# Kernel optimization log

Hardware: AMD Instinct MI355X
Metric: run time of the kernel (lower is better)

Reference implementation:

```python
import jax, jax.numpy as jnp
import numpy as np

D_MODEL = 1024
NUM_HEADS = 16
ROPE_THETA = 10000.0


def setup_inputs() -> dict:
    key = jax.random.key(0)
    ks = jax.random.split(key, 5)
    B, S, D = 4, 2048, D_MODEL
    std = (2.0 / (D * D)) ** 0.5
    return {
        "x": jax.random.normal(ks[0], (B, S, D), dtype=jnp.float32),
        "Wq": jax.random.normal(ks[1], (D, D), dtype=jnp.float32) * std,
        "Wk": jax.random.normal(ks[2], (D, D), dtype=jnp.float32) * std,
        "Wv": jax.random.normal(ks[3], (D, D), dtype=jnp.float32) * std,
        "Wo": jax.random.normal(ks[4], (D, D), dtype=jnp.float32) * std,
    }


def _apply_rope(t, sin, cos):
    # t: [B, H, S, d_k]; sin/cos: [S, d_k//2] (broadcast over B, H)
    e = t[..., 0::2]
    o = t[..., 1::2]
    rot = jnp.stack((e * cos - o * sin, e * sin + o * cos), axis=-1)
    return rot.reshape(t.shape)  # interleave back to d_k


def reference(x, Wq, Wk, Wv, Wo):
    B, S, D = x.shape
    H = NUM_HEADS
    dk = D // H

    def proj(W):
        y = jnp.einsum('bsd,ed->bse', x, W)  # Linear: weight is [out, in]
        return y.reshape(B, S, H, dk).transpose(0, 2, 1, 3)  # [B,H,S,dk]

    q, k, v = proj(Wq), proj(Wk), proj(Wv)

    # RoPE cache (token_positions = arange(S))
    half = dk // 2
    inv_freq = 1.0 / (ROPE_THETA ** (jnp.arange(half, dtype=jnp.float32) * 2.0 / dk))
    angles = jnp.arange(S, dtype=jnp.float32)[:, None] * inv_freq[None, :]  # [S, half]
    sin, cos = jnp.sin(angles), jnp.cos(angles)
    q = _apply_rope(q, sin, cos)
    k = _apply_rope(k, sin, cos)

    # scaled dot-product attention with causal mask
    scores = jnp.einsum('bhqd,bhkd->bhqk', q, k) / jnp.sqrt(jnp.float32(dk))
    causal = jnp.tril(jnp.ones((S, S), dtype=bool))
    scores = jnp.where(causal, scores, jnp.finfo(scores.dtype).min)
    p = jax.nn.softmax(scores, axis=-1)
    out = jnp.einsum('bhqk,bhkd->bhqd', p, v)  # [B,H,S,dk]

    out = out.transpose(0, 2, 1, 3).reshape(B, S, D)
    return jnp.einsum('bsd,ed->bse', out, Wo)
```

## Files before the change

kernel.cpp:

```cpp
#include <hip/hip_runtime.h>

typedef unsigned short u16;
typedef unsigned int   u32;

typedef short    short8 __attribute__((ext_vector_type(8)));
typedef __bf16   bf16x8 __attribute__((ext_vector_type(8)));
typedef _Float16 half8  __attribute__((ext_vector_type(8)));
typedef float    f32x4  __attribute__((ext_vector_type(4)));

#define S_LEN   2048
#define DM      1024
#define NHEAD   16
#define DK      64
#define BH_TOT  64
#define M_TOK   8192
#define KDIM    1024

__device__ __forceinline__ u16 f2bf(float f) {
    u32 u = __builtin_bit_cast(u32, f);
    u += 0x7FFFu + ((u >> 16) & 1u);
    return (u16)(u >> 16);
}
__device__ __forceinline__ float bf2f(u16 h) {
    u32 u = ((u32)h) << 16;
    return __builtin_bit_cast(float, u);
}
__device__ __forceinline__ f32x4 mfma_bf16(short8 a, short8 b, f32x4 c) {
    return __builtin_amdgcn_mfma_f32_16x16x32_bf16(
        __builtin_bit_cast(bf16x8, a), __builtin_bit_cast(bf16x8, b), c, 0, 0, 0);
}
__device__ __forceinline__ f32x4 mfma_f16(half8 a, half8 b, f32x4 c) {
    return __builtin_amdgcn_mfma_f32_16x16x32_f16(a, b, c, 0, 0, 0);
}
__device__ __forceinline__ u32 pk_f16(float a, float b) {
    return __builtin_bit_cast(u32, __builtin_amdgcn_cvt_pkrtz(a, b));
}
__device__ __forceinline__ void gl_lds16(const void* g, void* l) {
    __builtin_amdgcn_global_load_lds(
        (const __attribute__((address_space(1))) u32*)g,
        (__attribute__((address_space(3))) u32*)l, 16, 0, 0);
}
__device__ __forceinline__ void bar_raw() { asm volatile("s_barrier" ::: "memory"); }
__device__ __forceinline__ void wait_vm4() { asm volatile("s_waitcnt vmcnt(4)" ::: "memory"); }
__device__ __forceinline__ void wait_vm0() { asm volatile("s_waitcnt vmcnt(0)" ::: "memory"); }

__device__ __forceinline__ int perm_inv(int rc) {
    const int nt = rc >> 4, mid = (rc >> 2) & 3, r = rc & 3;
    return 32 * (nt >> 1) + 8 * mid + 4 * (nt & 1) + r;
}

__global__ void cvt_all(const float4* __restrict__ x,  const float4* __restrict__ Wq,
                        const float4* __restrict__ Wk, const float4* __restrict__ Wv,
                        const float4* __restrict__ Wo,
                        uint2* __restrict__ oX, uint2* __restrict__ oWcat,
                        uint2* __restrict__ oWo) {
    const int i = blockIdx.x * 256 + threadIdx.x;
    const float4* in;
    uint2* out;
    if (i < 2097152) {
        in = x + i;  out = oX + i;
    } else {
        const int j = i - 2097152;
        const int w = j >> 18, k = j & 262143;
        in  = (w == 0 ? Wq : w == 1 ? Wk : w == 2 ? Wv : Wo) + k;
        out = (w < 3) ? (oWcat + w * 262144 + k) : (oWo + k);
    }
    float4 f = *in;
    uint2 o;
    o.x = (u32)f2bf(f.x) | ((u32)f2bf(f.y) << 16);
    o.y = (u32)f2bf(f.z) | ((u32)f2bf(f.w) << 16);
    *out = o;
}

template <int MODE>
__global__ __launch_bounds__(256)
void gemm_nt(const u16* __restrict__ A, const u16* __restrict__ Bw,
             u16* __restrict__ oQ, u16* __restrict__ oK, u16* __restrict__ oVt,
             float* __restrict__ oF) {
    __shared__ u16 As[2][128 * 32];
    __shared__ u16 Bs[2][128 * 32];
    const int tid  = threadIdx.x;
    const int wave = tid >> 6, lane = tid & 63;
    const int quad = lane >> 4, l15 = lane & 15;
    const int wr = wave >> 1, wc = wave & 1;
    const int mbase = blockIdx.y * 128;
    const int nbase = blockIdx.x * 128;

    f32x4 acc[4][4];
#pragma unroll
    for (int i = 0; i < 4; i++)
#pragma unroll
        for (int j = 0; j < 4; j++) acc[i][j] = (f32x4)0.0f;

    const int srow0 = wave * 32 + (lane >> 2);
    const int srow1 = srow0 + 16;
    const int scolb = ((lane & 3) ^ ((lane >> 3) & 3)) * 16;
    const int ldsOff = wave * 2048 + lane * 16;
    const u16* gA0 = A  + (size_t)(mbase + srow0) * KDIM;
    const u16* gA1 = A  + (size_t)(mbase + srow1) * KDIM;
    const u16* gB0 = Bw + (size_t)(nbase + srow0) * KDIM;
    const u16* gB1 = Bw + (size_t)(nbase + srow1) * KDIM;
    const int koffq = (quad ^ ((l15 >> 1) & 3)) * 8;

    gl_lds16((const char*)gA0 + scolb, (char*)As[0] + ldsOff);
    gl_lds16((const char*)gA1 + scolb, (char*)As[0] + ldsOff + 1024);
    gl_lds16((const char*)gB0 + scolb, (char*)Bs[0] + ldsOff);
    gl_lds16((const char*)gB1 + scolb, (char*)Bs[0] + ldsOff + 1024);

    const int KT = KDIM / 32;
    for (int kt = 0; kt < KT; kt++) {
        const int cur = kt & 1, nxt = cur ^ 1;
        const int kkn = ((kt + 1 < KT) ? (kt + 1) : kt) * 32;
        bar_raw();
        gl_lds16((const char*)(gA0 + kkn) + scolb, (char*)As[nxt] + ldsOff);
        gl_lds16((const char*)(gA1 + kkn) + scolb, (char*)As[nxt] + ldsOff + 1024);
        gl_lds16((const char*)(gB0 + kkn) + scolb, (char*)Bs[nxt] + ldsOff);
        gl_lds16((const char*)(gB1 + kkn) + scolb, (char*)Bs[nxt] + ldsOff + 1024);
        wait_vm4();
        bar_raw();

        short8 af[4], bf[4];
#pragma unroll
        for (int mt = 0; mt < 4; mt++)
            af[mt] = *(const short8*)&As[cur][(wr * 64 + mt * 16 + l15) * 32 + koffq];
#pragma unroll
        for (int nt = 0; nt < 4; nt++)
            bf[nt] = *(const short8*)&Bs[cur][(wc * 64 + nt * 16 + l15) * 32 + koffq];
#pragma unroll
        for (int mt = 0; mt < 4; mt++)
#pragma unroll
            for (int nt = 0; nt < 4; nt++)
                acc[mt][nt] = mfma_bf16(af[mt], bf[nt], acc[mt][nt]);
    }
    wait_vm0();

    const int proj_blk = (MODE == 0) ? (nbase >> 10) : 2;

    float fq[4], cf[4], sf[4];
    if (MODE == 0 && proj_blk < 2) {
#pragma unroll
        for (int nt = 0; nt < 4; nt++) {
            const float fi = __expf(-(float)(nt * 8 + (l15 >> 1)) * 0.287823136624255f);
            fq[nt] = fi;
            cf[nt] = cosf(fi);
            sf[nt] = sinf(fi);
        }
    }
    const int par = l15 & 1;

#pragma unroll
    for (int mt = 0; mt < 4; mt++) {
#pragma unroll
        for (int nt = 0; nt < 4; nt++) {
            const int n  = nbase + wc * 64 + nt * 16 + l15;
            const int mb = mbase + wr * 64 + mt * 16 + quad * 4;
            f32x4 v = acc[mt][nt];
            if (MODE == 0) {
                const int e = n & 1023;
                const int h = e >> 6, d = e & 63;
                if (proj_blk == 2) {
                    const int b_ = mb >> 11, s = mb & 2047;
                    const int bh = b_ * NHEAD + h;
                    uint2 pk;
                    pk.x = pk_f16(v[0], v[1]);
                    pk.y = pk_f16(v[2], v[3]);
                    *(uint2*)&oVt[((size_t)bh * DK + d) * S_LEN + s] = pk;
                } else {
                    u16* dst = (proj_blk == 0) ? oQ : oK;
                    float vp[4];
#pragma unroll
                    for (int r = 0; r < 4; r++) vp[r] = __shfl_xor(v[r], 1);
                    const int b_ = mb >> 11, s0 = mb & 2047;
                    const int bh = b_ * NHEAD + h;
                    float cc = cosf((float)s0 * fq[nt]);
                    float ss = sinf((float)s0 * fq[nt]);
#pragma unroll
                    for (int r = 0; r < 4; r++) {
                        const float res = par ? (vp[r] * ss + v[r] * cc)
                                              : (v[r] * cc - vp[r] * ss);
                        dst[((size_t)bh * S_LEN + (s0 + r)) * DK + d] = f2bf(res);
                        const float c2 = cc * cf[nt] - ss * sf[nt];
                        ss = ss * cf[nt] + cc * sf[nt];
                        cc = c2;
                    }
                }
            } else {
#pragma unroll
                for (int r = 0; r < 4; r++)
                    oF[(size_t)(mb + r) * DM + n] = v[r];
            }
        }
    }
}

__global__ __launch_bounds__(256)
void flash_attn(const u16* __restrict__ Q, const u16* __restrict__ K,
                const u16* __restrict__ Vt, u16* __restrict__ Oc) {
    __shared__ u16 Ks[2][64 * 64];
    __shared__ u16 Vs[2][64 * 64];
    const int qt = 31 - (int)blockIdx.y;
    const int bh = blockIdx.x;
    const int tid  = threadIdx.x;
    const int wave = tid >> 6, lane = tid & 63;
    const int quad = lane >> 4, l15 = lane & 15;
    const int x7 = l15 & 7;
    const size_t headQK = (size_t)bh * S_LEN * DK;
    const size_t headVt = (size_t)bh * DK * S_LEN;
    const int b = bh >> 4, h = bh & 15;
    const float SCL = 0.18033688011112042f;

    half8 ones;
#pragma unroll
    for (int j = 0; j < 8; j++) ones[j] = (_Float16)1.0f;

    const int rwl  = lane >> 3;
    const int scol = (lane & 7) ^ rwl;
    const int rc0 = wave * 16 + rwl, rc1 = rc0 + 8;
    const u16* gK0 = K  + headQK + (size_t)perm_inv(rc0) * DK + scol * 8;
    const u16* gK1 = K  + headQK + (size_t)perm_inv(rc1) * DK + scol * 8;
    const u16* gV0 = Vt + headVt + (size_t)rc0 * S_LEN + scol * 8;
    const u16* gV1 = Vt + headVt + (size_t)rc1 * S_LEN + scol * 8;
    const int ldsOff = wave * 2048 + lane * 16;
    const int koff0 = (quad ^ x7) * 8;
    const int koff1 = ((4 + quad) ^ x7) * 8;

    const int qrow = qt * 64 + wave * 16 + l15;
    const short8 qf0 = *(const short8*)&Q[headQK + (size_t)qrow * DK + quad * 8];
    const short8 qf1 = *(const short8*)&Q[headQK + (size_t)qrow * DK + 32 + quad * 8];

    float m_st = -__builtin_inff();
    f32x4 lacc = (f32x4)0.0f;
    f32x4 oacc[4];
#pragma unroll
    for (int n = 0; n < 4; n++) oacc[n] = (f32x4)0.0f;

    gl_lds16(gK0, (char*)Ks[0] + ldsOff);
    gl_lds16(gK1, (char*)Ks[0] + ldsOff + 1024);
    gl_lds16(gV0, (char*)Vs[0] + ldsOff);
    gl_lds16(gV1, (char*)Vs[0] + ldsOff + 1024);

    for (int kt = 0; kt <= qt; kt++) {
        const int cur = kt & 1, nxt = cur ^ 1;
        bar_raw();
        {
            const int ktn = (kt < qt) ? kt + 1 : qt;
            gl_lds16(gK0 + (size_t)ktn * 64 * DK, (char*)Ks[nxt] + ldsOff);
            gl_lds16(gK1 + (size_t)ktn * 64 * DK, (char*)Ks[nxt] + ldsOff + 1024);
            gl_lds16(gV0 + ktn * 64,              (char*)Vs[nxt] + ldsOff);
            gl_lds16(gV1 + ktn * 64,              (char*)Vs[nxt] + ldsOff + 1024);
        }
        wait_vm4();
        bar_raw();

        f32x4 sc[4];
#pragma unroll
        for (int nt = 0; nt < 4; nt++) {
            const int rb = (nt * 16 + l15) * 64;
            short8 kf0 = *(const short8*)&Ks[cur][rb + koff0];
            short8 kf1 = *(const short8*)&Ks[cur][rb + koff1];
            f32x4 z = (f32x4)0.0f;
            z = mfma_bf16(kf0, qf0, z);
            z = mfma_bf16(kf1, qf1, z);
#pragma unroll
            for (int r = 0; r < 4; r++) z[r] *= SCL;
            sc[nt] = z;
        }
        if (kt == qt) {
            const int qloc = wave * 16 + l15;
#pragma unroll
            for (int nt = 0; nt < 4; nt++) {
                const int kb = 32 * (nt >> 1) + 8 * quad + 4 * (nt & 1);
#pragma unroll
                for (int r = 0; r < 4; r++)
                    if (kb + r > qloc) sc[nt][r] = -__builtin_inff();
            }
        }
        float mx0 = fmaxf(fmaxf(sc[0][0], sc[0][1]), fmaxf(sc[0][2], sc[0][3]));
        float mx1 = fmaxf(fmaxf(sc[1][0], sc[1][1]), fmaxf(sc[1][2], sc[1][3]));
        float mx2 = fmaxf(fmaxf(sc[2][0], sc[2][1]), fmaxf(sc[2][2], sc[2][3]));
        float mx3 = fmaxf(fmaxf(sc[3][0], sc[3][1]), fmaxf(sc[3][2], sc[3][3]));
        float mx = fmaxf(fmaxf(mx0, mx1), fmaxf(mx2, mx3));
        mx = fmaxf(mx, __shfl_xor(mx, 16));
        mx = fmaxf(mx, __shfl_xor(mx, 32));
        const float mn = fmaxf(m_st, mx);
        const float alpha = __builtin_amdgcn_exp2f(m_st - mn);
        m_st = mn;
#pragma unroll
        for (int nt = 0; nt < 4; nt++)
#pragma unroll
            for (int r = 0; r < 4; r++)
                sc[nt][r] = __builtin_amdgcn_exp2f(sc[nt][r] - m_st);
        u32 pw[8];
        pw[0] = pk_f16(sc[0][0], sc[0][1]); pw[1] = pk_f16(sc[0][2], sc[0][3]);
        pw[2] = pk_f16(sc[1][0], sc[1][1]); pw[3] = pk_f16(sc[1][2], sc[1][3]);
        pw[4] = pk_f16(sc[2][0], sc[2][1]); pw[5] = pk_f16(sc[2][2], sc[2][3]);
        pw[6] = pk_f16(sc[3][0], sc[3][1]); pw[7] = pk_f16(sc[3][2], sc[3][3]);
        half8 pf0 = __builtin_bit_cast(half8, *(uint4*)&pw[0]);
        half8 pf1 = __builtin_bit_cast(half8, *(uint4*)&pw[4]);
        float alr[4];
#pragma unroll
        for (int r = 0; r < 4; r++) alr[r] = __shfl(alpha, quad * 20 + r);
#pragma unroll
        for (int n = 0; n < 4; n++)
#pragma unroll
            for (int r = 0; r < 4; r++) oacc[n][r] *= alr[r];
#pragma unroll
        for (int r = 0; r < 4; r++) lacc[r] *= alr[r];
#pragma unroll
        for (int c = 0; c < 2; c++) {
            const half8 pf = c ? pf1 : pf0;
            lacc = mfma_f16(pf, ones, lacc);
            const int voff = ((c * 4 + quad) ^ x7) * 8;
#pragma unroll
            for (int nt2 = 0; nt2 < 4; nt2++) {
                half8 vf = __builtin_bit_cast(half8,
                    *(const short8*)&Vs[cur][(nt2 * 16 + l15) * 64 + voff]);
                oacc[nt2] = mfma_f16(pf, vf, oacc[nt2]);
            }
        }
    }
    wait_vm0();

#pragma unroll
    for (int r = 0; r < 4; r++) {
        const float inv = 1.0f / lacc[r];
        const int s = qt * 64 + wave * 16 + quad * 4 + r;
#pragma unroll
        for (int nt2 = 0; nt2 < 4; nt2++)
            Oc[((size_t)(b * S_LEN + s)) * DM + h * 64 + nt2 * 16 + l15] =
                f2bf(oacc[nt2][r] * inv);
    }
}

#define OFF_XBF  ((size_t)0)
#define OFF_WCAT ((size_t)8388608)
#define OFF_WO   ((size_t)11534336)
#define OFF_QB   ((size_t)12582912)
#define OFF_KB   ((size_t)20971520)
#define OFF_VT   ((size_t)29360128)

extern "C" void kernel_launch(void* const* d_in, const int* in_sizes, int n_in,
                              void* d_out, int out_size, void* d_ws, size_t ws_size,
                              hipStream_t stream) {
    const float* x  = (const float*)d_in[0];
    const float* Wq = (const float*)d_in[1];
    const float* Wk = (const float*)d_in[2];
    const float* Wv = (const float*)d_in[3];
    const float* Wo = (const float*)d_in[4];
    u16* ws  = (u16*)d_ws;
    u16* XBF = ws + OFF_XBF;
    u16* WCA = ws + OFF_WCAT;
    u16* WOB = ws + OFF_WO;
    u16* QB  = ws + OFF_QB;
    u16* KB  = ws + OFF_KB;
    u16* VT  = ws + OFF_VT;
    u16* AT  = XBF;

    cvt_all<<<12288, 256, 0, stream>>>((const float4*)x, (const float4*)Wq,
                                       (const float4*)Wk, (const float4*)Wv,
                                       (const float4*)Wo,
                                       (uint2*)XBF, (uint2*)WCA, (uint2*)WOB);

    gemm_nt<0><<<dim3(24, 64), 256, 0, stream>>>(XBF, WCA, QB, KB, VT, nullptr);
    flash_attn<<<dim3(64, 32), 256, 0, stream>>>(QB, KB, VT, AT);
    gemm_nt<1><<<dim3(8, 64), 256, 0, stream>>>(AT, WOB, nullptr, nullptr, nullptr,
                                                (float*)d_out);
}
```

Measured before the change: 277.2 us.

## Process two query tiles per flash block and precompute RoPE sin/cos table

Each flash-attention block now handles 128 query rows as two 64-row halves that share every K/V tile loaded into LDS. This halves the grid and the number of K/V loads per query. Separately, the RoPE sin/cos values are precomputed into a workspace table inside the conversion kernel, and the QKV GEMM epilogue loads them instead of running the sin/cos recurrence. The trade-offs are higher register pressure from doubled accumulators, fewer blocks for causal load balancing, and extra global reads in the epilogue.

```diff
diff --git a/kernel.cpp b/kernel.cpp
--- a/kernel.cpp
+++ b/kernel.cpp
@@ -21,10 +21,6 @@
     u += 0x7FFFu + ((u >> 16) & 1u);
     return (u16)(u >> 16);
 }
-__device__ __forceinline__ float bf2f(u16 h) {
-    u32 u = ((u32)h) << 16;
-    return __builtin_bit_cast(float, u);
-}
 __device__ __forceinline__ f32x4 mfma_bf16(short8 a, short8 b, f32x4 c) {
     return __builtin_amdgcn_mfma_f32_16x16x32_bf16(
         __builtin_bit_cast(bf16x8, a), __builtin_bit_cast(bf16x8, b), c, 0, 0, 0);
@@ -53,30 +49,40 @@
                         const float4* __restrict__ Wk, const float4* __restrict__ Wv,
                         const float4* __restrict__ Wo,
                         uint2* __restrict__ oX, uint2* __restrict__ oWcat,
-                        uint2* __restrict__ oWo) {
+                        uint2* __restrict__ oWo,
+                        float* __restrict__ sT, float* __restrict__ cT) {
     const int i = blockIdx.x * 256 + threadIdx.x;
-    const float4* in;
-    uint2* out;
-    if (i < 2097152) {
-        in = x + i;  out = oX + i;
+    if (i < 3145728) {
+        const float4* in;
+        uint2* out;
+        if (i < 2097152) {
+            in = x + i;  out = oX + i;
+        } else {
+            const int j = i - 2097152;
+            const int w = j >> 18, k = j & 262143;
+            in  = (w == 0 ? Wq : w == 1 ? Wk : w == 2 ? Wv : Wo) + k;
+            out = (w < 3) ? (oWcat + w * 262144 + k) : (oWo + k);
+        }
+        float4 f = *in;
+        uint2 o;
+        o.x = (u32)f2bf(f.x) | ((u32)f2bf(f.y) << 16);
+        o.y = (u32)f2bf(f.z) | ((u32)f2bf(f.w) << 16);
+        *out = o;
     } else {
-        const int j = i - 2097152;
-        const int w = j >> 18, k = j & 262143;
-        in  = (w == 0 ? Wq : w == 1 ? Wk : w == 2 ? Wv : Wo) + k;
-        out = (w < 3) ? (oWcat + w * 262144 + k) : (oWo + k);
-    }
-    float4 f = *in;
-    uint2 o;
-    o.x = (u32)f2bf(f.x) | ((u32)f2bf(f.y) << 16);
-    o.y = (u32)f2bf(f.z) | ((u32)f2bf(f.w) << 16);
-    *out = o;
+        const int idx = i - 3145728;
+        const float fi = expf(-(float)(idx >> 11) * 0.287823136624255f);
+        const float ang = (float)(idx & 2047) * fi;
+        sT[idx] = sinf(ang);
+        cT[idx] = cosf(ang);
+    }
 }
 
 template <int MODE>
 __global__ __launch_bounds__(256)
 void gemm_nt(const u16* __restrict__ A, const u16* __restrict__ Bw,
              u16* __restrict__ oQ, u16* __restrict__ oK, u16* __restrict__ oVt,
-             float* __restrict__ oF) {
+             float* __restrict__ oF,
+             const float* __restrict__ ropeS, const float* __restrict__ ropeC) {
     __shared__ u16 As[2][128 * 32];
     __shared__ u16 Bs[2][128 * 32];
     const int tid  = threadIdx.x;
@@ -136,14 +142,14 @@
 
     const int proj_blk = (MODE == 0) ? (nbase >> 10) : 2;
 
-    float fq[4], cf[4], sf[4];
+    const float* sB[4];
+    const float* cB[4];
     if (MODE == 0 && proj_blk < 2) {
 #pragma unroll
         for (int nt = 0; nt < 4; nt++) {
-            const float fi = __expf(-(float)(nt * 8 + (l15 >> 1)) * 0.287823136624255f);
-            fq[nt] = fi;
-            cf[nt] = cosf(fi);
-            sf[nt] = sinf(fi);
+            const int fi = nt * 8 + (l15 >> 1);
+            sB[nt] = ropeS + fi * 2048;
+            cB[nt] = ropeC + fi * 2048;
         }
     }
     const int par = l15 & 1;
@@ -172,16 +178,13 @@
                     for (int r = 0; r < 4; r++) vp[r] = __shfl_xor(v[r], 1);
                     const int b_ = mb >> 11, s0 = mb & 2047;
                     const int bh = b_ * NHEAD + h;
-                    float cc = cosf((float)s0 * fq[nt]);
-                    float ss = sinf((float)s0 * fq[nt]);
+                    const f32x4 sn = *(const f32x4*)(sB[nt] + s0);
+                    const f32x4 cs = *(const f32x4*)(cB[nt] + s0);
 #pragma unroll
                     for (int r = 0; r < 4; r++) {
-                        const float res = par ? (vp[r] * ss + v[r] * cc)
-                                              : (v[r] * cc - vp[r] * ss);
+                        const float res = par ? (vp[r] * sn[r] + v[r] * cs[r])
+                                              : (v[r] * cs[r] - vp[r] * sn[r]);
                         dst[((size_t)bh * S_LEN + (s0 + r)) * DK + d] = f2bf(res);
-                        const float c2 = cc * cf[nt] - ss * sf[nt];
-                        ss = ss * cf[nt] + cc * sf[nt];
-                        cc = c2;
                     }
                 }
             } else {
@@ -198,7 +201,7 @@
                 const u16* __restrict__ Vt, u16* __restrict__ Oc) {
     __shared__ u16 Ks[2][64 * 64];
     __shared__ u16 Vs[2][64 * 64];
-    const int qt = 31 - (int)blockIdx.y;
+    const int qt = 15 - (int)blockIdx.y;
     const int bh = blockIdx.x;
     const int tid  = threadIdx.x;
     const int wave = tid >> 6, lane = tid & 63;
@@ -224,26 +227,36 @@
     const int koff0 = (quad ^ x7) * 8;
     const int koff1 = ((4 + quad) ^ x7) * 8;
 
-    const int qrow = qt * 64 + wave * 16 + l15;
-    const short8 qf0 = *(const short8*)&Q[headQK + (size_t)qrow * DK + quad * 8];
-    const short8 qf1 = *(const short8*)&Q[headQK + (size_t)qrow * DK + 32 + quad * 8];
-
-    float m_st = -__builtin_inff();
-    f32x4 lacc = (f32x4)0.0f;
-    f32x4 oacc[4];
-#pragma unroll
-    for (int n = 0; n < 4; n++) oacc[n] = (f32x4)0.0f;
-
+    short8 qf[2][2];
+#pragma unroll
+    for (int hh = 0; hh < 2; hh++) {
+        const int qrow = qt * 128 + hh * 64 + wave * 16 + l15;
+        qf[hh][0] = *(const short8*)&Q[headQK + (size_t)qrow * DK + quad * 8];
+        qf[hh][1] = *(const short8*)&Q[headQK + (size_t)qrow * DK + 32 + quad * 8];
+    }
+
+    float m_st[2];
+    f32x4 lacc[2];
+    f32x4 oacc[2][4];
+#pragma unroll
+    for (int hh = 0; hh < 2; hh++) {
+        m_st[hh] = -__builtin_inff();
+        lacc[hh] = (f32x4)0.0f;
+#pragma unroll
+        for (int n = 0; n < 4; n++) oacc[hh][n] = (f32x4)0.0f;
+    }
+
+    const int NT = 2 * qt + 2;
     gl_lds16(gK0, (char*)Ks[0] + ldsOff);
     gl_lds16(gK1, (char*)Ks[0] + ldsOff + 1024);
     gl_lds16(gV0, (char*)Vs[0] + ldsOff);
     gl_lds16(gV1, (char*)Vs[0] + ldsOff + 1024);
 
-    for (int kt = 0; kt <= qt; kt++) {
+    for (int kt = 0; kt < NT; kt++) {
         const int cur = kt & 1, nxt = cur ^ 1;
         bar_raw();
         {
-            const int ktn = (kt < qt) ? kt + 1 : qt;
+            const int ktn = (kt + 1 < NT) ? kt + 1 : kt;
             gl_lds16(gK0 + (size_t)ktn * 64 * DK, (char*)Ks[nxt] + ldsOff);
             gl_lds16(gK1 + (size_t)ktn * 64 * DK, (char*)Ks[nxt] + ldsOff + 1024);
             gl_lds16(gV0 + ktn * 64,              (char*)Vs[nxt] + ldsOff);
@@ -252,92 +265,100 @@
         wait_vm4();
         bar_raw();
 
-        f32x4 sc[4];
-#pragma unroll
-        for (int nt = 0; nt < 4; nt++) {
-            const int rb = (nt * 16 + l15) * 64;
-            short8 kf0 = *(const short8*)&Ks[cur][rb + koff0];
-            short8 kf1 = *(const short8*)&Ks[cur][rb + koff1];
-            f32x4 z = (f32x4)0.0f;
-            z = mfma_bf16(kf0, qf0, z);
-            z = mfma_bf16(kf1, qf1, z);
-#pragma unroll
-            for (int r = 0; r < 4; r++) z[r] *= SCL;
-            sc[nt] = z;
-        }
-        if (kt == qt) {
-            const int qloc = wave * 16 + l15;
+#pragma unroll
+        for (int hh = 0; hh < 2; hh++) {
+            if (hh == 0 && kt == 2 * qt + 1) continue;
+            f32x4 sc[4];
 #pragma unroll
             for (int nt = 0; nt < 4; nt++) {
-                const int kb = 32 * (nt >> 1) + 8 * quad + 4 * (nt & 1);
+                const int rb = (nt * 16 + l15) * 64;
+                short8 kf0 = *(const short8*)&Ks[cur][rb + koff0];
+                short8 kf1 = *(const short8*)&Ks[cur][rb + koff1];
+                f32x4 z = (f32x4)0.0f;
+                z = mfma_bf16(kf0, qf[hh][0], z);
+                z = mfma_bf16(kf1, qf[hh][1], z);
+#pragma unroll
+                for (int r = 0; r < 4; r++) z[r] *= SCL;
+                sc[nt] = z;
+            }
+            if (kt == 2 * qt + hh) {
+                const int qloc = wave * 16 + l15;
+#pragma unroll
+                for (int nt = 0; nt < 4; nt++) {
+                    const int kb = 32 * (nt >> 1) + 8 * quad + 4 * (nt & 1);
+#pragma unroll
+                    for (int r = 0; r < 4; r++)
+                        if (kb + r > qloc) sc[nt][r] = -__builtin_inff();
+                }
+            }
+            float mx0 = fmaxf(fmaxf(sc[0][0], sc[0][1]), fmaxf(sc[0][2], sc[0][3]));
+            float mx1 = fmaxf(fmaxf(sc[1][0], sc[1][1]), fmaxf(sc[1][2], sc[1][3]));
+            float mx2 = fmaxf(fmaxf(sc[2][0], sc[2][1]), fmaxf(sc[2][2], sc[2][3]));
+            float mx3 = fmaxf(fmaxf(sc[3][0], sc[3][1]), fmaxf(sc[3][2], sc[3][3]));
+            float mx = fmaxf(fmaxf(mx0, mx1), fmaxf(mx2, mx3));
+            mx = fmaxf(mx, __shfl_xor(mx, 16));
+            mx = fmaxf(mx, __shfl_xor(mx, 32));
+            const float mn = fmaxf(m_st[hh], mx);
+            const float alpha = __builtin_amdgcn_exp2f(m_st[hh] - mn);
+            m_st[hh] = mn;
+#pragma unroll
+            for (int nt = 0; nt < 4; nt++)
 #pragma unroll
                 for (int r = 0; r < 4; r++)
-                    if (kb + r > qloc) sc[nt][r] = -__builtin_inff();
+                    sc[nt][r] = __builtin_amdgcn_exp2f(sc[nt][r] - m_st[hh]);
+            u32 pw[8];
+            pw[0] = pk_f16(sc[0][0], sc[0][1]); pw[1] = pk_f16(sc[0][2], sc[0][3]);
+            pw[2] = pk_f16(sc[1][0], sc[1][1]); pw[3] = pk_f16(sc[1][2], sc[1][3]);
+            pw[4] = pk_f16(sc[2][0], sc[2][1]); pw[5] = pk_f16(sc[2][2], sc[2][3]);
+            pw[6] = pk_f16(sc[3][0], sc[3][1]); pw[7] = pk_f16(sc[3][2], sc[3][3]);
+            half8 pf0 = __builtin_bit_cast(half8, *(uint4*)&pw[0]);
+            half8 pf1 = __builtin_bit_cast(half8, *(uint4*)&pw[4]);
+            float alr[4];
+#pragma unroll
+            for (int r = 0; r < 4; r++) alr[r] = __shfl(alpha, quad * 20 + r);
+#pragma unroll
+            for (int n = 0; n < 4; n++)
+#pragma unroll
+                for (int r = 0; r < 4; r++) oacc[hh][n][r] *= alr[r];
+#pragma unroll
+            for (int r = 0; r < 4; r++) lacc[hh][r] *= alr[r];
+#pragma unroll
+            for (int c = 0; c < 2; c++) {
+                const half8 pf = c ? pf1 : pf0;
+                lacc[hh] = mfma_f16(pf, ones, lacc[hh]);
+                const int voff = ((c * 4 + quad) ^ x7) * 8;
+#pragma unroll
+                for (int nt2 = 0; nt2 < 4; nt2++) {
+                    half8 vf = __builtin_bit_cast(half8,
+                        *(const short8*)&Vs[cur][(nt2 * 16 + l15) * 64 + voff]);
+                    oacc[hh][nt2] = mfma_f16(pf, vf, oacc[hh][nt2]);
+                }
             }
         }
-        float mx0 = fmaxf(fmaxf(sc[0][0], sc[0][1]), fmaxf(sc[0][2], sc[0][3]));
-        float mx1 = fmaxf(fmaxf(sc[1][0], sc[1][1]), fmaxf(sc[1][2], sc[1][3]));
-        float mx2 = fmaxf(fmaxf(sc[2][0], sc[2][1]), fmaxf(sc[2][2], sc[2][3]));
-        float mx3 = fmaxf(fmaxf(sc[3][0], sc[3][1]), fmaxf(sc[3][2], sc[3][3]));
-        float mx = fmaxf(fmaxf(mx0, mx1), fmaxf(mx2, mx3));
-        mx = fmaxf(mx, __shfl_xor(mx, 16));
-        mx = fmaxf(mx, __shfl_xor(mx, 32));
-        const float mn = fmaxf(m_st, mx);
-        const float alpha = __builtin_amdgcn_exp2f(m_st - mn);
-        m_st = mn;
-#pragma unroll
-        for (int nt = 0; nt < 4; nt++)
-#pragma unroll
-            for (int r = 0; r < 4; r++)
-                sc[nt][r] = __builtin_amdgcn_exp2f(sc[nt][r] - m_st);
-        u32 pw[8];
-        pw[0] = pk_f16(sc[0][0], sc[0][1]); pw[1] = pk_f16(sc[0][2], sc[0][3]);
-        pw[2] = pk_f16(sc[1][0], sc[1][1]); pw[3] = pk_f16(sc[1][2], sc[1][3]);
-        pw[4] = pk_f16(sc[2][0], sc[2][1]); pw[5] = pk_f16(sc[2][2], sc[2][3]);
-        pw[6] = pk_f16(sc[3][0], sc[3][1]); pw[7] = pk_f16(sc[3][2], sc[3][3]);
-        half8 pf0 = __builtin_bit_cast(half8, *(uint4*)&pw[0]);
-        half8 pf1 = __builtin_bit_cast(half8, *(uint4*)&pw[4]);
-        float alr[4];
-#pragma unroll
-        for (int r = 0; r < 4; r++) alr[r] = __shfl(alpha, quad * 20 + r);
-#pragma unroll
-        for (int n = 0; n < 4; n++)
-#pragma unroll
-            for (int r = 0; r < 4; r++) oacc[n][r] *= alr[r];
-#pragma unroll
-        for (int r = 0; r < 4; r++) lacc[r] *= alr[r];
-#pragma unroll
-        for (int c = 0; c < 2; c++) {
-            const half8 pf = c ? pf1 : pf0;
-            lacc = mfma_f16(pf, ones, lacc);
-            const int voff = ((c * 4 + quad) ^ x7) * 8;
-#pragma unroll
-            for (int nt2 = 0; nt2 < 4; nt2++) {
-                half8 vf = __builtin_bit_cast(half8,
-                    *(const short8*)&Vs[cur][(nt2 * 16 + l15) * 64 + voff]);
-                oacc[nt2] = mfma_f16(pf, vf, oacc[nt2]);
-            }
-        }
     }
     wait_vm0();
 
 #pragma unroll
-    for (int r = 0; r < 4; r++) {
-        const float inv = 1.0f / lacc[r];
-        const int s = qt * 64 + wave * 16 + quad * 4 + r;
-#pragma unroll
-        for (int nt2 = 0; nt2 < 4; nt2++)
-            Oc[((size_t)(b * S_LEN + s)) * DM + h * 64 + nt2 * 16 + l15] =
-                f2bf(oacc[nt2][r] * inv);
-    }
-}
-
-#define OFF_XBF  ((size_t)0)
-#define OFF_WCAT ((size_t)8388608)
-#define OFF_WO   ((size_t)11534336)
-#define OFF_QB   ((size_t)12582912)
-#define OFF_KB   ((size_t)20971520)
-#define OFF_VT   ((size_t)29360128)
+    for (int hh = 0; hh < 2; hh++) {
+#pragma unroll
+        for (int r = 0; r < 4; r++) {
+            const float inv = 1.0f / lacc[hh][r];
+            const int s = qt * 128 + hh * 64 + wave * 16 + quad * 4 + r;
+#pragma unroll
+            for (int nt2 = 0; nt2 < 4; nt2++)
+                Oc[((size_t)(b * S_LEN + s)) * DM + h * 64 + nt2 * 16 + l15] =
+                    f2bf(oacc[hh][nt2][r] * inv);
+        }
+    }
+}
+
+#define OFF_XBF   ((size_t)0)
+#define OFF_WCAT  ((size_t)8388608)
+#define OFF_WO    ((size_t)11534336)
+#define OFF_QB    ((size_t)12582912)
+#define OFF_KB    ((size_t)20971520)
+#define OFF_VT    ((size_t)29360128)
+#define OFF_ROPE  ((size_t)37748736)
 
 extern "C" void kernel_launch(void* const* d_in, const int* in_sizes, int n_in,
                               void* d_out, int out_size, void* d_ws, size_t ws_size,
@@ -354,15 +375,19 @@
     u16* QB  = ws + OFF_QB;
     u16* KB  = ws + OFF_KB;
     u16* VT  = ws + OFF_VT;
+    float* ropeS = (float*)(ws + OFF_ROPE);
+    float* ropeC = ropeS + 65536;
     u16* AT  = XBF;
 
-    cvt_all<<<12288, 256, 0, stream>>>((const float4*)x, (const float4*)Wq,
+    cvt_all<<<12544, 256, 0, stream>>>((const float4*)x, (const float4*)Wq,
                                        (const float4*)Wk, (const float4*)Wv,
                                        (const float4*)Wo,
-                                       (uint2*)XBF, (uint2*)WCA, (uint2*)WOB);
-
-    gemm_nt<0><<<dim3(24, 64), 256, 0, stream>>>(XBF, WCA, QB, KB, VT, nullptr);
-    flash_attn<<<dim3(64, 32), 256, 0, stream>>>(QB, KB, VT, AT);
+                                       (uint2*)XBF, (uint2*)WCA, (uint2*)WOB,
+                                       ropeS, ropeC);
+
+    gemm_nt<0><<<dim3(24, 64), 256, 0, stream>>>(XBF, WCA, QB, KB, VT, nullptr,
+                                                 ropeS, ropeC);
+    flash_attn<<<dim3(64, 16), 256, 0, stream>>>(QB, KB, VT, AT);
     gemm_nt<1><<<dim3(8, 64), 256, 0, stream>>>(AT, WOB, nullptr, nullptr, nullptr,
-                                                (float*)d_out);
-}
+                                                (float*)d_out, nullptr, nullptr);
+}
```

After: 269.4 us. 2.8% less time.
